# Kernel tuning notes

Measured on AMD Instinct MI355X. Metric: run time of the kernel, lower is better.

## Reference

```python
import jax, jax.numpy as jnp
import numpy as np

TOP_K = 4


def setup_inputs() -> dict:
    key = jax.random.key(0)
    ks = jax.random.split(key, 8)
    B, S, D, I, E = 4, 2048, 1024, 512, 16
    scale = 0.05  # keep activations numerically sane (torch init uses raw randn)
    return {
        "x": jax.random.normal(ks[0], (B, S, D), dtype=jnp.float32),
        "router_w": jax.random.normal(ks[1], (E, D), dtype=jnp.float32) * scale,
        "w1_w": jax.random.normal(ks[2], (E, I, D), dtype=jnp.float32) * scale,
        "w1_b": jax.random.normal(ks[3], (E, I), dtype=jnp.float32) * scale,
        "w2_w": jax.random.normal(ks[4], (E, D, I), dtype=jnp.float32) * scale,
        "w2_b": jax.random.normal(ks[5], (E, D), dtype=jnp.float32) * scale,
        "w3_w": jax.random.normal(ks[6], (E, I, D), dtype=jnp.float32) * scale,
        "w3_b": jax.random.normal(ks[7], (E, I), dtype=jnp.float32) * scale,
    }


def reference(x, router_w, w1_w, w1_b, w2_w, w2_b, w3_w, w3_b):
    B, S, D = x.shape
    E = router_w.shape[0]
    K = TOP_K
    # router: softmax over experts, then top-k
    scores = jax.nn.softmax(jnp.einsum('bsd,ed->bse', x, router_w), axis=-1)
    top_scores, sel = jax.lax.top_k(scores, K)            # [B,S,K]
    sel_flat = sel.reshape(B, S * K)                      # flattened expert ids
    ts_flat = top_scores.reshape(B, S * K)
    # stable argsort by expert id -> dispatch order
    idxs = jnp.argsort(sel_flat, axis=-1, stable=True)    # [B, S*K]
    ts = jnp.take_along_axis(ts_flat, idxs, axis=-1)      # [B, S*K]
    tok = idxs // K                                       # source token index
    # gather tokens into dispatch order
    xs = jnp.take_along_axis(x, tok[:, :, None], axis=1)  # [B, S*K, D]
    T = (S * K) // E                                      # tokens per expert (fixed)
    xs = xs.reshape(B, E, T, D).transpose(1, 0, 2, 3).reshape(E, B * T, D)
    h1 = jnp.einsum('end,eid->eni', xs, w1_w) + w1_b[:, None, :]
    h3 = jnp.einsum('end,eid->eni', xs, w3_w) + w3_b[:, None, :]
    h = jax.nn.silu(h1) * h3
    out = jnp.einsum('eni,edi->end', h, w2_w) + w2_b[:, None, :]  # [E, B*T, D]
    # un-permute back to [B, S*K, D], weight by router scores
    out = out.reshape(E, B, T, D).transpose(1, 0, 2, 3).reshape(B, S * K, D)
    out = out * ts[:, :, None]
    # scatter-add combine back to token positions
    res = jax.vmap(lambda t, o: jnp.zeros((S, D), x.dtype).at[t].add(o))(tok, out)
    return res
```

## Files before the change

kernel.cpp:

```cpp
#include <hip/hip_runtime.h>

typedef _Float16 f16;
typedef f16 f16x8 __attribute__((ext_vector_type(8)));
typedef float f32x4 __attribute__((ext_vector_type(4)));

#define B_ 4
#define S_ 2048
#define D_ 1024
#define I_ 512
#define E_ 16
#define K_ 4
#define TPB_ 8192
#define EROWS_ 2048

__device__ __forceinline__ void gload16(const void* g, void* l) {
    __builtin_amdgcn_global_load_lds(
        (const __attribute__((address_space(1))) void*)g,
        (__attribute__((address_space(3))) void*)l, 16, 0, 0);
}

__device__ __forceinline__ int xcd_swz(int bid, int nwg) {
    int cpx = nwg >> 3;
    return (bid & 7) * cpx + (bid >> 3);
}

__device__ __forceinline__ void cvt8(const float* __restrict__ s, f16* __restrict__ d, int i) {
    const float4* sp = (const float4*)s;
    float4 a = sp[2 * i], b = sp[2 * i + 1];
    f16x8 v;
    v[0] = (f16)a.x; v[1] = (f16)a.y; v[2] = (f16)a.z; v[3] = (f16)a.w;
    v[4] = (f16)b.x; v[5] = (f16)b.y; v[6] = (f16)b.z; v[7] = (f16)b.w;
    *(f16x8*)(d + (size_t)i * 8) = v;
}

__global__ void k_convert(const float* __restrict__ x, const float* __restrict__ w1,
                          const float* __restrict__ w3, const float* __restrict__ w2,
                          f16* __restrict__ xh, f16* __restrict__ w1h,
                          f16* __restrict__ w3h, f16* __restrict__ w2h) {
    const int N8 = (B_ * S_ * D_) / 8;
    int stride = gridDim.x * blockDim.x;
    for (int i = blockIdx.x * blockDim.x + threadIdx.x; i < N8; i += stride) {
        cvt8(x, xh, i);
        cvt8(w1, w1h, i);
        cvt8(w3, w3h, i);
        cvt8(w2, w2h, i);
    }
}

__global__ void k_router(const float* __restrict__ x, const float* __restrict__ rw,
                         int* __restrict__ sel, float* __restrict__ ts) {
    int w = threadIdx.x >> 6, lane = threadIdx.x & 63;
    int tok = blockIdx.x * 4 + w;
    const float4* xp = (const float4*)(x + (size_t)tok * D_);
    float xr[16];
    #pragma unroll
    for (int j = 0; j < 4; ++j) {
        float4 v = xp[lane * 4 + j];
        xr[j * 4 + 0] = v.x; xr[j * 4 + 1] = v.y; xr[j * 4 + 2] = v.z; xr[j * 4 + 3] = v.w;
    }
    float sc[E_];
    #pragma unroll
    for (int e = 0; e < E_; ++e) {
        const float4* wp = (const float4*)(rw + (size_t)e * D_);
        float a = 0.f;
        #pragma unroll
        for (int j = 0; j < 4; ++j) {
            float4 v = wp[lane * 4 + j];
            a += xr[j * 4 + 0] * v.x + xr[j * 4 + 1] * v.y + xr[j * 4 + 2] * v.z + xr[j * 4 + 3] * v.w;
        }
        #pragma unroll
        for (int off = 32; off; off >>= 1) a += __shfl_xor(a, off);
        sc[e] = a;
    }
    float mx = sc[0];
    #pragma unroll
    for (int e = 1; e < E_; ++e) mx = fmaxf(mx, sc[e]);
    float ex[E_]; float sum = 0.f;
    #pragma unroll
    for (int e = 0; e < E_; ++e) { ex[e] = __expf(sc[e] - mx); sum += ex[e]; }
    float inv = 1.f / sum;
    if (lane == 0) {
        unsigned usedMask = 0;
        #pragma unroll
        for (int k = 0; k < K_; ++k) {
            int bi = -1; float bv = -1e30f, bev = 0.f;
            #pragma unroll
            for (int e = 0; e < E_; ++e) {
                bool ok = !((usedMask >> e) & 1) && (sc[e] > bv);
                if (ok) { bv = sc[e]; bi = e; bev = ex[e]; }
            }
            usedMask |= 1u << bi;
            sel[(size_t)tok * K_ + k] = bi;
            ts[(size_t)tok * K_ + k] = bev * inv;
        }
    }
}

__global__ void k_sort(const int* __restrict__ sel, const float* __restrict__ ts,
                       int* __restrict__ src_tok, float* __restrict__ gate) {
    __shared__ int ssel[TPB_];
    __shared__ int scnt[E_];
    int b = blockIdx.x, tid = threadIdx.x;
    for (int i = 0; i < 8; ++i) ssel[i * 1024 + tid] = sel[(size_t)b * TPB_ + i * 1024 + tid];
    __syncthreads();
    int e = tid >> 6, lane = tid & 63;
    unsigned long long lm = (1ull << lane) - 1ull;
    int c = 0;
    for (int ch = 0; ch < 128; ++ch) {
        unsigned long long m = __ballot(ssel[ch * 64 + lane] == e);
        c += __popcll(m);
    }
    if (lane == 0) scnt[e] = c;
    __syncthreads();
    int run = 0;
    for (int i = 0; i < E_; ++i) run += (i < e) ? scnt[i] : 0;
    for (int ch = 0; ch < 128; ++ch) {
        int f = ch * 64 + lane;
        int s = ssel[f];
        unsigned long long m = __ballot(s == e);
        if (s == e) {
            int p = run + __popcll(m & lm);
            src_tok[(size_t)b * TPB_ + p] = f >> 2;
            gate[(size_t)b * TPB_ + p] = ts[(size_t)b * TPB_ + f];
        }
        run += __popcll(m);
    }
}

__global__ __launch_bounds__(256, 2) void k_gemm1(
    const f16* __restrict__ xh, const f16* __restrict__ w1h, const f16* __restrict__ w3h,
    const float* __restrict__ b1, const float* __restrict__ b3,
    const int* __restrict__ src_tok, f16* __restrict__ h) {
    __shared__ f16 Als[128 * 64];
    __shared__ f16 B1s[128 * 64];
    __shared__ f16 B3s[128 * 64];
    int bid = xcd_swz(blockIdx.x, 1024);
    int e = bid >> 6, rem = bid & 63, mb = rem >> 2, nb = rem & 3;
    int tid = threadIdx.x, lane = tid & 63, w = tid >> 6, wr = w >> 1, wc = w & 1;

    int lr = lane >> 3;
    int cswz = (lane & 7) ^ lr;
    const f16* arow[4];
    int bofs[4];
    int ldsA[4];
    #pragma unroll
    for (int i = 0; i < 4; ++i) {
        int r = w * 32 + i * 8 + lr;
        int re = mb * 128 + r;
        int bb = re >> 9;
        int tokk = src_tok[bb * TPB_ + e * 512 + (re & 511)];
        arow[i] = xh + ((size_t)(bb * S_ + tokk)) * D_ + cswz * 8;
        int brw = nb * 128 + r;
        bofs[i] = (e * I_ + brw) * D_ + cswz * 8;
        ldsA[i] = w * 2048 + i * 512;
    }

    f32x4 acc1[4][4], acc3[4][4];
    const f32x4 fz = {0.f, 0.f, 0.f, 0.f};
    #pragma unroll
    for (int m = 0; m < 4; ++m)
        #pragma unroll
        for (int n = 0; n < 4; ++n) { acc1[m][n] = fz; acc3[m][n] = fz; }

    for (int ks = 0; ks < 16; ++ks) {
        __syncthreads();
        int ko = ks * 64;
        #pragma unroll
        for (int i = 0; i < 4; ++i) {
            gload16(arow[i] + ko, &Als[ldsA[i]]);
            gload16(w1h + bofs[i] + ko, &B1s[ldsA[i]]);
            gload16(w3h + bofs[i] + ko, &B3s[ldsA[i]]);
        }
        __syncthreads();
        #pragma unroll
        for (int kk = 0; kk < 2; ++kk) {
            f16x8 af[4], bf1[4], bf3[4];
            int kb = kk * 32 + (lane >> 4) * 8;
            #pragma unroll
            for (int m = 0; m < 4; ++m) {
                int row = wr * 64 + m * 16 + (lane & 15);
                af[m] = *(const f16x8*)&Als[row * 64 + (kb ^ ((row & 7) * 8))];
            }
            #pragma unroll
            for (int n = 0; n < 4; ++n) {
                int row = wc * 64 + n * 16 + (lane & 15);
                int o = row * 64 + (kb ^ ((row & 7) * 8));
                bf1[n] = *(const f16x8*)&B1s[o];
                bf3[n] = *(const f16x8*)&B3s[o];
            }
            #pragma unroll
            for (int m = 0; m < 4; ++m)
                #pragma unroll
                for (int n = 0; n < 4; ++n) {
                    acc1[m][n] = __builtin_amdgcn_mfma_f32_16x16x32_f16(af[m], bf1[n], acc1[m][n], 0, 0, 0);
                    acc3[m][n] = __builtin_amdgcn_mfma_f32_16x16x32_f16(af[m], bf3[n], acc3[m][n], 0, 0, 0);
                }
        }
    }
    int icb = nb * 128 + wc * 64;
    float bias1[4], bias3[4];
    #pragma unroll
    for (int n = 0; n < 4; ++n) {
        int ic = icb + n * 16 + (lane & 15);
        bias1[n] = b1[e * I_ + ic];
        bias3[n] = b3[e * I_ + ic];
    }
    #pragma unroll
    for (int m = 0; m < 4; ++m)
        #pragma unroll
        for (int n = 0; n < 4; ++n) {
            int col = icb + n * 16 + (lane & 15);
            #pragma unroll
            for (int r = 0; r < 4; ++r) {
                float z1 = acc1[m][n][r] + bias1[n];
                float z3 = acc3[m][n][r] + bias3[n];
                float sv = z1 / (1.f + __expf(-z1));
                float hv = sv * z3;
                int row = mb * 128 + wr * 64 + m * 16 + (lane >> 4) * 4 + r;
                h[((size_t)e * EROWS_ + row) * I_ + col] = (f16)hv;
            }
        }
}

__global__ __launch_bounds__(256, 2) void k_gemm2(
    const f16* __restrict__ h, const f16* __restrict__ w2h, const float* __restrict__ b2,
    const int* __restrict__ src_tok, const float* __restrict__ gate, float* __restrict__ out) {
    __shared__ f16 Als[128 * 64];
    __shared__ f16 Bs[128 * 64];
    int bid = xcd_swz(blockIdx.x, 2048);
    int e = bid >> 7, rem = bid & 127, mb = rem >> 3, nb = rem & 7;
    int tid = threadIdx.x, lane = tid & 63, w = tid >> 6, wr = w >> 1, wc = w & 1;

    int lr = lane >> 3;
    int cswz = (lane & 7) ^ lr;
    size_t aofs[4], bofs[4];
    int ldsA[4];
    #pragma unroll
    for (int i = 0; i < 4; ++i) {
        int r = w * 32 + i * 8 + lr;
        aofs[i] = ((size_t)e * EROWS_ + mb * 128 + r) * I_ + cswz * 8;
        bofs[i] = ((size_t)e * D_ + nb * 128 + r) * I_ + cswz * 8;
        ldsA[i] = w * 2048 + i * 512;
    }

    f32x4 acc[4][4];
    const f32x4 fz = {0.f, 0.f, 0.f, 0.f};
    #pragma unroll
    for (int m = 0; m < 4; ++m)
        #pragma unroll
        for (int n = 0; n < 4; ++n) acc[m][n] = fz;

    for (int ks = 0; ks < 8; ++ks) {
        __syncthreads();
        int ko = ks * 64;
        #pragma unroll
        for (int i = 0; i < 4; ++i) {
            gload16(h + aofs[i] + ko, &Als[ldsA[i]]);
            gload16(w2h + bofs[i] + ko, &Bs[ldsA[i]]);
        }
        __syncthreads();
        #pragma unroll
        for (int kk = 0; kk < 2; ++kk) {
            f16x8 af[4], bf[4];
            int kb = kk * 32 + (lane >> 4) * 8;
            #pragma unroll
            for (int m = 0; m < 4; ++m) {
                int row = wr * 64 + m * 16 + (lane & 15);
                af[m] = *(const f16x8*)&Als[row * 64 + (kb ^ ((row & 7) * 8))];
            }
            #pragma unroll
            for (int n = 0; n < 4; ++n) {
                int row = wc * 64 + n * 16 + (lane & 15);
                bf[n] = *(const f16x8*)&Bs[row * 64 + (kb ^ ((row & 7) * 8))];
            }
            #pragma unroll
            for (int m = 0; m < 4; ++m)
                #pragma unroll
                for (int n = 0; n < 4; ++n)
                    acc[m][n] = __builtin_amdgcn_mfma_f32_16x16x32_f16(af[m], bf[n], acc[m][n], 0, 0, 0);
        }
    }
    int dcb = nb * 128 + wc * 64;
    float bias[4];
    #pragma unroll
    for (int n = 0; n < 4; ++n) bias[n] = b2[e * D_ + dcb + n * 16 + (lane & 15)];
    #pragma unroll
    for (int m = 0; m < 4; ++m)
        #pragma unroll
        for (int r = 0; r < 4; ++r) {
            int re = mb * 128 + wr * 64 + m * 16 + (lane >> 4) * 4 + r;
            int bb = re >> 9;
            int pos = bb * TPB_ + e * 512 + (re & 511);
            int tokk = src_tok[pos];
            float g = gate[pos];
            float* op = out + ((size_t)(bb * S_ + tokk)) * D_;
            #pragma unroll
            for (int n = 0; n < 4; ++n) {
                int col = dcb + n * 16 + (lane & 15);
                atomicAdd(op + col, g * (acc[m][n][r] + bias[n]));
            }
        }
}

extern "C" void kernel_launch(void* const* d_in, const int* in_sizes, int n_in,
                              void* d_out, int out_size, void* d_ws, size_t ws_size,
                              hipStream_t stream) {
    const float* x  = (const float*)d_in[0];
    const float* rw = (const float*)d_in[1];
    const float* w1 = (const float*)d_in[2];
    const float* b1 = (const float*)d_in[3];
    const float* w2 = (const float*)d_in[4];
    const float* b2 = (const float*)d_in[5];
    const float* w3 = (const float*)d_in[6];
    const float* b3 = (const float*)d_in[7];
    float* out = (float*)d_out;

    const size_t NEL = (size_t)B_ * S_ * D_;
    char* p = (char*)d_ws;
    f16* xh  = (f16*)p; p += NEL * 2;
    f16* w1h = (f16*)p; p += NEL * 2;
    f16* w3h = (f16*)p; p += NEL * 2;
    f16* w2h = (f16*)p; p += NEL * 2;
    f16* h   = (f16*)p; p += (size_t)E_ * EROWS_ * I_ * 2;
    int*   sel     = (int*)p;   p += (size_t)B_ * TPB_ * 4;
    float* ts      = (float*)p; p += (size_t)B_ * TPB_ * 4;
    int*   src_tok = (int*)p;   p += (size_t)B_ * TPB_ * 4;
    float* gate    = (float*)p; p += (size_t)B_ * TPB_ * 4;

    hipMemsetAsync(d_out, 0, (size_t)out_size * sizeof(float), stream);
    k_convert<<<2048, 256, 0, stream>>>(x, w1, w3, w2, xh, w1h, w3h, w2h);
    k_router<<<2048, 256, 0, stream>>>(x, rw, sel, ts);
    k_sort<<<4, 1024, 0, stream>>>(sel, ts, src_tok, gate);
    k_gemm1<<<1024, 256, 0, stream>>>(xh, w1h, w3h, b1, b3, src_tok, h);
    k_gemm2<<<2048, 256, 0, stream>>>(h, w2h, b2, src_tok, gate, out);
}
```

Baseline: 431.8 us.

## Replace atomic scatter-add combine with fp16 staging buffer and gather-combine kernel

The second GEMM now writes its per-expert outputs as fp16 into a staging buffer instead of scattering gated fp32 atomics into the output. A new combine kernel uses an inverse-permutation map from the sort to gather each token's four expert rows, weight them by router scores and write the output once, so the output memset is no longer needed. This removes atomic contention and read-modify-write traffic but adds a 64 MB fp16 intermediate written and read back, and rounds the expert outputs to fp16 before the weighted sum. An atomic fallback path is kept for when the workspace is too small.

```diff
diff --git a/kernel.cpp b/kernel.cpp
--- a/kernel.cpp
+++ b/kernel.cpp
@@ -96,8 +96,8 @@
     }
 }
 
-__global__ void k_sort(const int* __restrict__ sel, const float* __restrict__ ts,
-                       int* __restrict__ src_tok, float* __restrict__ gate) {
+__global__ void k_sort(const int* __restrict__ sel, int* __restrict__ src_tok,
+                       int* __restrict__ invp) {
     __shared__ int ssel[TPB_];
     __shared__ int scnt[E_];
     int b = blockIdx.x, tid = threadIdx.x;
@@ -121,7 +121,7 @@
         if (s == e) {
             int p = run + __popcll(m & lm);
             src_tok[(size_t)b * TPB_ + p] = f >> 2;
-            gate[(size_t)b * TPB_ + p] = ts[(size_t)b * TPB_ + f];
+            invp[(size_t)b * TPB_ + f] = p;
         }
         run += __popcll(m);
     }
@@ -224,7 +224,7 @@
 
 __global__ __launch_bounds__(256, 2) void k_gemm2(
     const f16* __restrict__ h, const f16* __restrict__ w2h, const float* __restrict__ b2,
-    const int* __restrict__ src_tok, const float* __restrict__ gate, float* __restrict__ out) {
+    f16* __restrict__ h2p) {
     __shared__ f16 Als[128 * 64];
     __shared__ f16 Bs[128 * 64];
     int bid = xcd_swz(blockIdx.x, 2048);
@@ -288,11 +288,89 @@
     for (int m = 0; m < 4; ++m)
         #pragma unroll
         for (int r = 0; r < 4; ++r) {
+            int row = mb * 128 + wr * 64 + m * 16 + (lane >> 4) * 4 + r;
+            #pragma unroll
+            for (int n = 0; n < 4; ++n) {
+                int col = dcb + n * 16 + (lane & 15);
+                h2p[((size_t)e * EROWS_ + row) * D_ + col] = (f16)(acc[m][n][r] + bias[n]);
+            }
+        }
+}
+
+__global__ __launch_bounds__(256, 2) void k_gemm2_atomic(
+    const f16* __restrict__ h, const f16* __restrict__ w2h, const float* __restrict__ b2,
+    const int* __restrict__ src_tok, const int* __restrict__ invp,
+    const float* __restrict__ ts, float* __restrict__ out) {
+    __shared__ f16 Als[128 * 64];
+    __shared__ f16 Bs[128 * 64];
+    int bid = xcd_swz(blockIdx.x, 2048);
+    int e = bid >> 7, rem = bid & 127, mb = rem >> 3, nb = rem & 7;
+    int tid = threadIdx.x, lane = tid & 63, w = tid >> 6, wr = w >> 1, wc = w & 1;
+
+    int lr = lane >> 3;
+    int cswz = (lane & 7) ^ lr;
+    size_t aofs[4], bofs[4];
+    int ldsA[4];
+    #pragma unroll
+    for (int i = 0; i < 4; ++i) {
+        int r = w * 32 + i * 8 + lr;
+        aofs[i] = ((size_t)e * EROWS_ + mb * 128 + r) * I_ + cswz * 8;
+        bofs[i] = ((size_t)e * D_ + nb * 128 + r) * I_ + cswz * 8;
+        ldsA[i] = w * 2048 + i * 512;
+    }
+    f32x4 acc[4][4];
+    const f32x4 fz = {0.f, 0.f, 0.f, 0.f};
+    #pragma unroll
+    for (int m = 0; m < 4; ++m)
+        #pragma unroll
+        for (int n = 0; n < 4; ++n) acc[m][n] = fz;
+    for (int ks = 0; ks < 8; ++ks) {
+        __syncthreads();
+        int ko = ks * 64;
+        #pragma unroll
+        for (int i = 0; i < 4; ++i) {
+            gload16(h + aofs[i] + ko, &Als[ldsA[i]]);
+            gload16(w2h + bofs[i] + ko, &Bs[ldsA[i]]);
+        }
+        __syncthreads();
+        #pragma unroll
+        for (int kk = 0; kk < 2; ++kk) {
+            f16x8 af[4], bf[4];
+            int kb = kk * 32 + (lane >> 4) * 8;
+            #pragma unroll
+            for (int m = 0; m < 4; ++m) {
+                int row = wr * 64 + m * 16 + (lane & 15);
+                af[m] = *(const f16x8*)&Als[row * 64 + (kb ^ ((row & 7) * 8))];
+            }
+            #pragma unroll
+            for (int n = 0; n < 4; ++n) {
+                int row = wc * 64 + n * 16 + (lane & 15);
+                bf[n] = *(const f16x8*)&Bs[row * 64 + (kb ^ ((row & 7) * 8))];
+            }
+            #pragma unroll
+            for (int m = 0; m < 4; ++m)
+                #pragma unroll
+                for (int n = 0; n < 4; ++n)
+                    acc[m][n] = __builtin_amdgcn_mfma_f32_16x16x32_f16(af[m], bf[n], acc[m][n], 0, 0, 0);
+        }
+    }
+    int dcb = nb * 128 + wc * 64;
+    float bias[4];
+    #pragma unroll
+    for (int n = 0; n < 4; ++n) bias[n] = b2[e * D_ + dcb + n * 16 + (lane & 15)];
+    #pragma unroll
+    for (int m = 0; m < 4; ++m)
+        #pragma unroll
+        for (int r = 0; r < 4; ++r) {
             int re = mb * 128 + wr * 64 + m * 16 + (lane >> 4) * 4 + r;
             int bb = re >> 9;
             int pos = bb * TPB_ + e * 512 + (re & 511);
             int tokk = src_tok[pos];
-            float g = gate[pos];
+            float g = 0.f;
+            #pragma unroll
+            for (int k = 0; k < K_; ++k)
+                if (invp[bb * TPB_ + tokk * K_ + k] == e * 512 + (re & 511))
+                    g = ts[bb * TPB_ + tokk * K_ + k];
             float* op = out + ((size_t)(bb * S_ + tokk)) * D_;
             #pragma unroll
             for (int n = 0; n < 4; ++n) {
@@ -300,6 +378,37 @@
                 atomicAdd(op + col, g * (acc[m][n][r] + bias[n]));
             }
         }
+}
+
+__global__ __launch_bounds__(256) void k_combine(
+    const f16* __restrict__ h2p, const float* __restrict__ ts,
+    const int* __restrict__ invp, float* __restrict__ out) {
+    int w = threadIdx.x >> 6, lane = threadIdx.x & 63;
+    int t = blockIdx.x * 4 + w;
+    int b = t >> 11, s = t & 2047;
+    int base = b * TPB_ + s * 4;
+    float g[4]; const f16* rows[4];
+    #pragma unroll
+    for (int k = 0; k < 4; ++k) {
+        int p = invp[base + k];
+        g[k] = ts[base + k];
+        int e = p >> 9, n = (b << 9) + (p & 511);
+        rows[k] = h2p + ((size_t)(e * EROWS_ + n)) * D_;
+    }
+    float* op = out + (size_t)t * D_;
+    #pragma unroll
+    for (int c = 0; c < 2; ++c) {
+        int d = c * 512 + lane * 8;
+        float a[8] = {0.f};
+        #pragma unroll
+        for (int k = 0; k < 4; ++k) {
+            f16x8 v = *(const f16x8*)(rows[k] + d);
+            #pragma unroll
+            for (int j = 0; j < 8; ++j) a[j] += g[k] * (float)v[j];
+        }
+        *(float4*)(op + d)     = make_float4(a[0], a[1], a[2], a[3]);
+        *(float4*)(op + d + 4) = make_float4(a[4], a[5], a[6], a[7]);
+    }
 }
 
 extern "C" void kernel_launch(void* const* d_in, const int* in_sizes, int n_in,
@@ -325,12 +434,19 @@
     int*   sel     = (int*)p;   p += (size_t)B_ * TPB_ * 4;
     float* ts      = (float*)p; p += (size_t)B_ * TPB_ * 4;
     int*   src_tok = (int*)p;   p += (size_t)B_ * TPB_ * 4;
-    float* gate    = (float*)p; p += (size_t)B_ * TPB_ * 4;
-
-    hipMemsetAsync(d_out, 0, (size_t)out_size * sizeof(float), stream);
+    int*   invp    = (int*)p;   p += (size_t)B_ * TPB_ * 4;
+    f16* h2p = (f16*)p; p += (size_t)E_ * EROWS_ * D_ * 2;
+    size_t need = (size_t)(p - (char*)d_ws);
+
     k_convert<<<2048, 256, 0, stream>>>(x, w1, w3, w2, xh, w1h, w3h, w2h);
     k_router<<<2048, 256, 0, stream>>>(x, rw, sel, ts);
-    k_sort<<<4, 1024, 0, stream>>>(sel, ts, src_tok, gate);
+    k_sort<<<4, 1024, 0, stream>>>(sel, src_tok, invp);
     k_gemm1<<<1024, 256, 0, stream>>>(xh, w1h, w3h, b1, b3, src_tok, h);
-    k_gemm2<<<2048, 256, 0, stream>>>(h, w2h, b2, src_tok, gate, out);
-}
+    if (ws_size >= need) {
+        k_gemm2<<<2048, 256, 0, stream>>>(h, w2h, b2, h2p);
+        k_combine<<<2048, 256, 0, stream>>>(h2p, ts, invp, out);
+    } else {
+        hipMemsetAsync(d_out, 0, (size_t)out_size * sizeof(float), stream);
+        k_gemm2_atomic<<<2048, 256, 0, stream>>>(h, w2h, b2, src_tok, invp, ts, out);
+    }
+}
```

After: 355.1 us. 17.8% less time.
